# Optimization experiments

Measured on AMD Instinct MI355X. Metric: run time of the kernel, lower is better.

## Reference

```python
import jax, jax.numpy as jnp
import numpy as np

E = 8            # num experts
CAP_FACTOR = 1.5
K_THRESH = 0.8
BAL_ALPHA = 0.005
REG_ALPHA = 1e-6
BN_EPS = 1e-5
POOL = 16


def setup_inputs() -> dict:
    key = jax.random.key(0)
    ks = jax.random.split(key, 8)
    B, H, L, D = 128, 1024, 512, 1024
    return {
        "x": jax.random.normal(ks[0], (B, H, L), jnp.float32),
        "conv_w": jax.random.normal(ks[1], (64, H, 3), jnp.float32) / np.float32(np.sqrt(3 * H)),
        "conv_b": jnp.zeros((64,), jnp.float32),
        "bn_gamma": jnp.ones((64 * POOL,), jnp.float32),
        "bn_beta": jnp.zeros((64 * POOL,), jnp.float32),
        "fc1_w": jax.random.normal(ks[2], (128, 64 * POOL), jnp.float32) / np.float32(np.sqrt(64 * POOL)),
        "fc1_b": jnp.zeros((128,), jnp.float32),
        "fc2_w": jax.random.normal(ks[3], (E, 128), jnp.float32) / np.float32(np.sqrt(128)),
        "fc2_b": jnp.zeros((E,), jnp.float32),
        "exp_w": jax.random.normal(ks[4], (E, H, D), jnp.float32) / np.float32(np.sqrt(H)),
        "exp_b": jnp.zeros((E, D), jnp.float32),
    }


def _forward(x, conv_w, conv_b, bn_gamma, bn_beta, fc1_w, fc1_b, fc2_w, fc2_b, exp_w, exp_b):
    B, H, L = x.shape
    # ---- router: Conv1d(H->64,k=3,p=1) -> GELU -> AdaptiveAvgPool1d(16) -> Flatten -> BN -> FC -> GELU -> FC -> softmax
    h = jax.lax.conv_general_dilated(x, conv_w, (1,), ((1, 1),),
                                     dimension_numbers=("NCH", "OIH", "NCH"))
    h = jax.nn.gelu(h + conv_b[None, :, None], approximate=False)          # [B,64,L]; torch GELU is exact erf
    h = h.reshape(B, 64, POOL, L // POOL).mean(-1).reshape(B, 64 * POOL)   # adaptive avg pool (L%16==0) + flatten
    mu, var = h.mean(0), h.var(0)                                          # training-mode (Sync)BatchNorm: batch stats
    h = (h - mu) / jnp.sqrt(var + BN_EPS) * bn_gamma + bn_beta
    h = jax.nn.gelu(h @ fc1_w.T + fc1_b, approximate=False)
    rw = jax.nn.softmax(h @ fc2_w.T + fc2_b, axis=1)                       # [B,E]; expert dropout = identity (eval)
    # ---- dynamic k: smallest k s.t. cumsum of sorted probs > threshold; only max over batch is used
    topk_w, topk_idx = jax.lax.top_k(rw, E)                                # full descending sort
    cum = jnp.cumsum(topk_w, axis=1)
    over = cum > K_THRESH
    k_per = jnp.where(jnp.any(over, axis=1), jnp.argmax(over, axis=1) + 1, E)
    max_k = jnp.max(jnp.clip(k_per, 1, E))
    col_valid = jnp.arange(E)[None, :] < max_k                             # broadcast [B,E]; cols >= max_k unused
    assign = jnp.where(col_valid, topk_idx, -1)
    # ---- capacity enforcement: per expert keep the `capacity` highest-weight assignments, drop the rest (-1)
    capacity = max(1, int(B * CAP_FACTOR / E))
    flat_idx, flat_w = assign.reshape(-1), topk_w.reshape(-1)              # row-major [B*E], matches torch flatten

    def keep_for_expert(e):
        m = flat_idx == e
        order = jnp.argsort(-jnp.where(m, flat_w, -jnp.inf))               # descending within expert e
        ranks = jnp.zeros_like(order).at[order].set(jnp.arange(order.shape[0]))
        return m & (ranks < capacity)

    keep = jax.vmap(keep_for_expert)(jnp.arange(E))                        # [E, B*E]
    counts = keep.sum(axis=1).astype(jnp.float32)                          # == bincount of valid final indices
    final_idx = jnp.where(jnp.any(keep, axis=0), flat_idx, -1).reshape(B, E)
    # ---- experts: mean-pool over length, per-expert Linear(H->D); gather each sample's selected experts
    pooled = x.mean(axis=2)                                                # [B,H]
    y = jnp.einsum("bh,ehd->bed", pooled, exp_w) + exp_b[None]             # [B,E,D] all-expert outputs
    outputs = jnp.take_along_axis(y, jnp.clip(final_idx, 0)[..., None], axis=1)
    outputs = jnp.where(final_idx[..., None] >= 0, outputs, 0.0)           # dropped slots contribute zeros
    # ---- combine: softmax over the max_k slots; dropped (-1) slots enter softmax with logit 0, as in torch
    logits = jnp.where(col_valid, topk_w * (final_idx >= 0), -jnp.inf)
    norm_w = jax.nn.softmax(logits, axis=1)                                # [B,E]
    pooler = jnp.einsum("bkd,bk->bd", outputs, norm_w)                     # [B,D]
    # ---- losses / stats
    usage = rw.mean(0)
    reg = jnp.sum(exp_w * exp_w) + jnp.sum(exp_b * exp_b)                  # sum ||param||_2^2 over expert params
    added_loss = BAL_ALPHA * jnp.var(usage, ddof=1) + REG_ALPHA * reg      # torch.var is unbiased
    return pooler, added_loss, usage, counts


def reference(x, conv_w, conv_b, bn_gamma, bn_beta, fc1_w, fc1_b, fc2_w, fc2_b, exp_w, exp_b):
    return _forward(x, conv_w, conv_b, bn_gamma, bn_beta, fc1_w, fc1_b, fc2_w, fc2_b, exp_w, exp_b)
```

## Files before the change

kernel.cpp:

```cpp
#include <hip/hip_runtime.h>
#include <hip/hip_bf16.h>
#include <math.h>

#define NB 128
#define NH 1024
#define NL 512
#define OC 64
#define NE 8
#define ND 1024
#define CAPACITY 24

static const size_t WS_PART  = 0;
static const size_t WS_WSEP  = 1048576;
static const size_t WS_PXT   = 2097152;
static const size_t WS_HPOOL = 2228224;
static const size_t WS_SCALE = 2359296;
static const size_t WS_SHIFT = 2360320;
static const size_t WS_A1    = 2361344;
static const size_t WS_TKW   = 2377728;
static const size_t WS_TKI   = 2378752;
static const size_t WS_USAGE = 2379784;
static const size_t WS_VARU  = 2379792;
static const size_t WS_REG   = 2379793;
static const size_t WS_CNT   = 2379794;
static const size_t WS_WMAT  = 2380832;
static const size_t WS_RW    = 2381856;
static const size_t WS_KP    = 2382880;

typedef __attribute__((ext_vector_type(8))) short bf16x8;
typedef __attribute__((ext_vector_type(4))) float f32x4;

__device__ __forceinline__ float gelu_exact(float v) {
    return 0.5f * v * (1.0f + erff(v * 0.70710678118654752440f));
}

__device__ __forceinline__ unsigned short f2bf_rne(float f) {
    unsigned int u = __float_as_uint(f);
    unsigned int r = u + 0x7FFFu + ((u >> 16) & 1u);
    return (unsigned short)(r >> 16);
}
__device__ __forceinline__ float bf2f(unsigned short h) {
    return __uint_as_float(((unsigned int)h) << 16);
}

__device__ __forceinline__ unsigned cvtpk_bf16(float a, float b) {
    unsigned r;
    asm("v_cvt_pk_bf16_f32 %0, %1, %2" : "=v"(r) : "v"(a), "v"(b));
    return r;
}

__global__ __launch_bounds__(256) void k_wsplit(const float* __restrict__ cw, float* __restrict__ ws)
{
    if (blockIdx.x == 0 && threadIdx.x == 0) ws[WS_REG] = 0.0f;
    unsigned short* wsep = (unsigned short*)(ws + WS_WSEP);
    int i = blockIdx.x * 256 + threadIdx.x;
    float v = cw[i];
    int j = i % 3;
    int t = i / 3;
    int h = t & 1023;
    int o = t >> 10;
    int it = h >> 5;
    int h5 = h & 31;
    int e = h5 & 7;
    int lane = (o & 15) | ((h5 >> 3) << 4);
    int mt = (o >> 4) & 3;
    unsigned short hi = f2bf_rne(v);
    unsigned short lo = f2bf_rne(v - bf2f(hi));
    size_t base = ((size_t)((it * 3 + j) * 4 + mt) * 2) * 512 + lane * 8 + e;
    wsep[base] = hi;
    wsep[base + 512] = lo;
}

__device__ __forceinline__ void cvt_unit(unsigned int* X, int lq, int h4,
                                         const float4* v, float* sh)
{
    sh[0] = sh[1] = sh[2] = sh[3] = 0.f;
#pragma unroll
    for (int i = 0; i < 4; ++i) {
        float a0 = ((const float*)&v[0])[i];
        float a1 = ((const float*)&v[1])[i];
        float a2 = ((const float*)&v[2])[i];
        float a3 = ((const float*)&v[3])[i];
        sh[0] += a0; sh[1] += a1; sh[2] += a2; sh[3] += a3;
        unsigned h01 = cvtpk_bf16(a0, a1);
        unsigned h23 = cvtpk_bf16(a2, a3);
        float r0 = a0 - __uint_as_float(h01 << 16);
        float r1 = a1 - __uint_as_float(h01 & 0xFFFF0000u);
        float r2 = a2 - __uint_as_float(h23 << 16);
        float r3 = a3 - __uint_as_float(h23 & 0xFFFF0000u);
        unsigned l01 = cvtpk_bf16(r0, r1);
        unsigned l23 = cvtpk_bf16(r2, r3);
        int r = lq * 4 + i;
        unsigned int* dst = X + r * 34 + ((2 * h4) ^ ((r & 3) << 2));
        *(uint2*)dst = make_uint2(h01, h23);
        *(uint2*)(dst + 16) = make_uint2(l01, l23);
    }
}

__global__ __launch_bounds__(256, 2) void k_convmfma(const float* __restrict__ x,
                                                     const float* __restrict__ cb,
                                                     float* __restrict__ ws)
{
    __shared__ unsigned int Xb[2][136 * 34];
    __shared__ float xs2[3][128];
    __shared__ float scb[64];

    const int lc = blockIdx.x, b = blockIdx.y;
    const int l0 = lc * 128;
    const int tid = threadIdx.x;
    const int wv = tid >> 6, lane = tid & 63;
    const int h4 = tid & 7;
    const int lqi = 1 + (tid >> 3);
    const bool has_halo = (tid < 16);
    const int lqh = (tid < 8) ? 0 : 33;
    const bool halo_ok = (tid < 8) ? (lc > 0) : (lc < 3);

    const unsigned short* wsg = (const unsigned short*)(ws + WS_WSEP);
    const float* xbase = x + (size_t)b * (NH * NL);
    float* poolp = ws + WS_PART + ((size_t)(lc * 128 + b)) * 1024;

    if (tid < 64) scb[tid] = cb[tid];

    f32x4 acc[4][2];
#pragma unroll
    for (int mt = 0; mt < 4; ++mt)
#pragma unroll
        for (int nt = 0; nt < 2; ++nt) acc[mt][nt] = (f32x4){0.f, 0.f, 0.f, 0.f};

    float4 xA[4], hA[4], xB[4], hB[4];

    auto xload = [&](int itL, float4* xc, float4* hc) {
        const int hn = itL * 32;
        const float* p = xbase + (size_t)(hn + h4 * 4) * NL + (l0 - 4 + lqi * 4);
#pragma unroll
        for (int jj = 0; jj < 4; ++jj) xc[jj] = *(const float4*)(p + jj * NL);
        if (has_halo) {
            int gl = l0 - 4 + lqh * 4;
#pragma unroll
            for (int jj = 0; jj < 4; ++jj)
                hc[jj] = halo_ok ? *(const float4*)(xbase + (size_t)(hn + h4 * 4 + jj) * NL + gl)
                                 : make_float4(0.f, 0.f, 0.f, 0.f);
        }
    };

    auto body = [&](int it, float4* xc, float4* hc) {
        unsigned int* Xw = Xb[it & 1];
        bf16x8 Ar[3][4][2];
        {
            const unsigned short* abase = wsg + (size_t)it * 12288 + lane * 8;
#pragma unroll
            for (int j = 0; j < 3; ++j)
#pragma unroll
                for (int mt = 0; mt < 4; ++mt) {
                    Ar[j][mt][0] = *(const bf16x8*)(abase + (size_t)(j * 8 + mt * 2) * 512);
                    Ar[j][mt][1] = *(const bf16x8*)(abase + (size_t)(j * 8 + mt * 2 + 1) * 512);
                }
        }
        {
            float sh[4];
            cvt_unit(Xw, lqi, h4, xc, sh);
#pragma unroll
            for (int jj = 0; jj < 4; ++jj) {
                float s = sh[jj];
                s += __shfl_xor(s, 8, 64);
                s += __shfl_xor(s, 16, 64);
                s += __shfl_xor(s, 32, 64);
                if ((lane >> 3) == 0) xs2[it % 3][wv * 32 + h4 * 4 + jj] = s;
            }
            if (has_halo) { float d[4]; cvt_unit(Xw, lqh, h4, hc, d); }
        }
        __syncthreads();
        if (it > 0 && tid < 32) {
            const float* S = xs2[(it - 1) % 3];
            poolp[(it - 1) * 32 + tid] = S[tid] + S[32 + tid] + S[64 + tid] + S[96 + tid];
        }
        if (it < 30) xload(it + 2, xc, hc);
        const int g4 = (lane >> 4) << 2;
#pragma unroll
        for (int j = 0; j < 3; ++j) {
            bf16x8 Bh[2], Bl[2];
#pragma unroll
            for (int nt = 0; nt < 2; ++nt) {
                int rx = 3 + j + wv * 32 + nt * 16 + (lane & 15);
                const unsigned int* bp = Xw + rx * 34 + (g4 ^ ((rx & 3) << 2));
                Bh[nt] = *(const bf16x8*)bp;
                Bl[nt] = *(const bf16x8*)(bp + 16);
            }
#pragma unroll
            for (int mt = 0; mt < 4; ++mt)
#pragma unroll
                for (int nt = 0; nt < 2; ++nt) {
                    acc[mt][nt] = __builtin_amdgcn_mfma_f32_16x16x32_bf16(Ar[j][mt][0], Bh[nt], acc[mt][nt], 0, 0, 0);
                    acc[mt][nt] = __builtin_amdgcn_mfma_f32_16x16x32_bf16(Ar[j][mt][0], Bl[nt], acc[mt][nt], 0, 0, 0);
                    acc[mt][nt] = __builtin_amdgcn_mfma_f32_16x16x32_bf16(Ar[j][mt][1], Bh[nt], acc[mt][nt], 0, 0, 0);
                }
        }
    };

    xload(0, xA, hA);
    xload(1, xB, hB);

    for (int it2 = 0; it2 < 32; it2 += 2) {
        body(it2, xA, hA);
        body(it2 + 1, xB, hB);
    }
    if (tid < 32) {
        const float* S = xs2[31 % 3];
        poolp[31 * 32 + tid] = S[tid] + S[32 + tid] + S[64 + tid] + S[96 + tid];
    }

    {
        const int g = lane >> 4, cidx = lane & 15;
#pragma unroll
        for (int mt = 0; mt < 4; ++mt) {
            float s[4];
#pragma unroll
            for (int r = 0; r < 4; ++r) {
                int o = mt * 16 + g * 4 + r;
                float bo = scb[o];
                s[r] = gelu_exact(acc[mt][0][r] + bo) + gelu_exact(acc[mt][1][r] + bo);
            }
#pragma unroll
            for (int m = 1; m < 16; m <<= 1) {
#pragma unroll
                for (int r = 0; r < 4; ++r) s[r] += __shfl_xor(s[r], m, 64);
            }
            if (cidx == 0) {
#pragma unroll
                for (int r = 0; r < 4; ++r) {
                    int o = mt * 16 + g * 4 + r;
                    ws[WS_HPOOL + (size_t)b * 1024 + o * 16 + lc * 4 + wv] = s[r] * (1.0f / 32.0f);
                }
            }
        }
    }
}

__global__ __launch_bounds__(256) void k_mid(const float* __restrict__ g,
                                             const float* __restrict__ bet,
                                             float* __restrict__ ws)
{
    int bx = blockIdx.x;
    if (bx < 512) {
        int id = bx * 256 + threadIdx.x;
        int b = id >> 10, h = id & 1023;
        float s = 0.0f;
#pragma unroll
        for (int lcc = 0; lcc < 4; lcc++) s += ws[WS_PART + ((size_t)(lcc * 128 + b)) * 1024 + h];
        ws[WS_PXT + (size_t)h * 128 + b] = s * (1.0f / 512.0f);
    } else {
        int f = (bx - 512) * 256 + threadIdx.x;
        const float* hp = ws + WS_HPOOL;
        float s = 0.0f;
        for (int b = 0; b < 128; b++) s += hp[(size_t)b * 1024 + f];
        float mu = s * (1.0f / 128.0f);
        float v = 0.0f;
        for (int b = 0; b < 128; b++) { float d = hp[(size_t)b * 1024 + f] - mu; v += d * d; }
        float var = v * (1.0f / 128.0f);
        float sc = g[f] / sqrtf(var + 1e-5f);
        ws[WS_SCALE + f] = sc;
        ws[WS_SHIFT + f] = bet[f] - mu * sc;
    }
}

__global__ __launch_bounds__(256) void k_fused(const float* __restrict__ w1,
                                               const float* __restrict__ b1,
                                               const float* __restrict__ w2,
                                               const float* __restrict__ b2,
                                               const float* __restrict__ ew,
                                               const float* __restrict__ eb,
                                               float* __restrict__ ws)
{
    __shared__ float smem[6400];
    const int bx = blockIdx.x;
    const int tid = threadIdx.x;

    if (bx < 256) {
        float* a_s = smem;
        float* b_s = smem + 4096;
        float* red2 = smem + 6144;
        const int e = bx >> 5, dt = (bx >> 1) & 15, ks = bx & 1;
        const int tb = tid >> 3, td = tid & 7;
        float acc[4][8];
#pragma unroll
        for (int i = 0; i < 4; i++)
#pragma unroll
            for (int j = 0; j < 8; j++) acc[i][j] = 0.0f;
        float ssq = 0.0f;

        const float* pxt = ws + WS_PXT;
        for (int kt = 0; kt < 512; kt += 32) {
            __syncthreads();
            for (int idx = tid; idx < 4096; idx += 256) {
                int kk = idx >> 7, bb = idx & 127;
                a_s[kk * 128 + bb] = pxt[(size_t)(ks * 512 + kt + kk) * 128 + bb];
            }
            for (int idx = tid; idx < 2048; idx += 256) {
                int kk = idx >> 6, d = idx & 63;
                float v = ew[(size_t)e * 1048576 + (size_t)(ks * 512 + kt + kk) * 1024 + dt * 64 + d];
                b_s[kk * 64 + d] = v;
                ssq += v * v;
            }
            __syncthreads();
#pragma unroll 4
            for (int kk = 0; kk < 32; kk++) {
                float4 av = *(const float4*)&a_s[kk * 128 + tb * 4];
                float4 b0 = *(const float4*)&b_s[kk * 64 + td * 8];
                float4 b1v = *(const float4*)&b_s[kk * 64 + td * 8 + 4];
                float aa[4] = {av.x, av.y, av.z, av.w};
                float bb4[8] = {b0.x, b0.y, b0.z, b0.w, b1v.x, b1v.y, b1v.z, b1v.w};
#pragma unroll
                for (int i = 0; i < 4; i++)
#pragma unroll
                    for (int j = 0; j < 8; j++) acc[i][j] = fmaf(aa[i], bb4[j], acc[i][j]);
            }
        }
        float* outp = ws + WS_PART + ((size_t)(ks * 8 + e) * 128) * 1024 + dt * 64;
#pragma unroll
        for (int i = 0; i < 4; i++) {
            int bb = tb * 4 + i;
            *(float4*)(outp + (size_t)bb * 1024 + td * 8) =
                make_float4(acc[i][0], acc[i][1], acc[i][2], acc[i][3]);
            *(float4*)(outp + (size_t)bb * 1024 + td * 8 + 4) =
                make_float4(acc[i][4], acc[i][5], acc[i][6], acc[i][7]);
        }
        if (bx == 0)
            for (int i = tid; i < 8192; i += 256) { float v = eb[i]; ssq += v * v; }
        red2[tid] = ssq;
        __syncthreads();
        for (int off = 128; off > 0; off >>= 1) {
            if (tid < off) red2[tid] += red2[tid + off];
            __syncthreads();
        }
        if (tid == 0) atomicAdd(ws + WS_REG, red2[0]);
    } else {
        float* hb  = smem;
        float* red = smem + 1024;
        float* ha  = smem + 1280;
        float* w2s = smem + 1408;
        float* lg  = smem + 2432;
        const int b = bx - 256;
        const float* hp = ws + WS_HPOOL + (size_t)b * 1024;
        for (int k = tid; k < 1024; k += 256)
            hb[k] = hp[k] * ws[WS_SCALE + k] + ws[WS_SHIFT + k];
        for (int i = tid; i < 1024; i += 256) w2s[i] = w2[i];
        __syncthreads();
        int o = tid & 127, kh = tid >> 7;
        const float4* wrp = (const float4*)(w1 + (size_t)o * 1024 + kh * 512);
        const float* hx = hb + kh * 512;
        float acc = 0.0f;
#pragma unroll 4
        for (int k = 0; k < 128; k++) {
            float4 w = wrp[k];
            acc = fmaf(hx[4 * k], w.x, acc);     acc = fmaf(hx[4 * k + 1], w.y, acc);
            acc = fmaf(hx[4 * k + 2], w.z, acc); acc = fmaf(hx[4 * k + 3], w.w, acc);
        }
        red[tid] = acc;
        __syncthreads();
        if (tid < 128)
            ha[tid] = gelu_exact(red[tid] + red[tid + 128] + b1[tid]);
        __syncthreads();
        if (tid < 8) {
            float a2 = b2[tid];
            for (int k = 0; k < 128; k++) a2 = fmaf(ha[k], w2s[tid * 128 + k], a2);
            lg[tid] = a2;
        }
        __syncthreads();
        if (tid == 0) {
            float rw[8];
            float m = -1e30f;
#pragma unroll
            for (int e = 0; e < 8; e++) m = fmaxf(m, lg[e]);
            float s = 0.0f;
#pragma unroll
            for (int e = 0; e < 8; e++) { rw[e] = expf(lg[e] - m); s += rw[e]; }
            float inv = 1.0f / s;
#pragma unroll
            for (int e = 0; e < 8; e++) { rw[e] *= inv; ws[WS_RW + b * 8 + e] = rw[e]; }
            float tw[8]; int ti[8]; unsigned used = 0;
#pragma unroll
            for (int r = 0; r < 8; r++) {
                float bv = -1e30f; int bi = 0;
#pragma unroll
                for (int e = 0; e < 8; e++) {
                    bool take = !((used >> e) & 1u) && (rw[e] > bv);
                    bv = take ? rw[e] : bv;
                    bi = take ? e : bi;
                }
                used |= (1u << bi);
                tw[r] = bv; ti[r] = bi;
            }
            float cum = 0.0f; int kp = 8;
#pragma unroll
            for (int r = 0; r < 8; r++) {
                cum += tw[r];
                if (cum > 0.8f) { kp = r + 1; break; }
            }
#pragma unroll
            for (int r = 0; r < 8; r++) {
                ws[WS_TKW + b * 8 + r] = tw[r];
                ((int*)ws)[WS_TKI + b * 8 + r] = ti[r];
            }
            ((int*)ws)[WS_KP + b] = kp;
        }
    }
}

__global__ __launch_bounds__(128) void k_route(float* __restrict__ ws)
{
    __shared__ float tkw_s[1024];
    __shared__ int   tki_s[1024];
    __shared__ int   keep_s[1024];
    __shared__ float wv_s[128];
    __shared__ int   sv_s[128];
    __shared__ float usg[8];
    __shared__ int   cnt_s[8];
    __shared__ int   mk;

    const int tid = threadIdx.x;
    const int b = tid;
    if (tid == 0) mk = 0;
    if (tid < 8) cnt_s[tid] = 0;
    __syncthreads();
    atomicMax(&mk, ((const int*)ws)[WS_KP + b]);
#pragma unroll
    for (int r = 0; r < 8; r++) {
        tkw_s[b * 8 + r] = ws[WS_TKW + b * 8 + r];
        tki_s[b * 8 + r] = ((const int*)ws)[WS_TKI + b * 8 + r];
    }
    __syncthreads();
    const int maxk = mk;

    if (tid < 8) {
        float s2 = 0.0f;
        for (int bb = 0; bb < 128; bb++) s2 += ws[WS_RW + bb * 8 + tid];
        float u = s2 * (1.0f / 128.0f);
        usg[tid] = u;
        ws[WS_USAGE + tid] = u;
    }
    __syncthreads();
    if (tid == 0) {
        float mu = 0.0f;
#pragma unroll
        for (int e = 0; e < 8; e++) mu += usg[e];
        mu *= (1.0f / 8.0f);
        float v = 0.0f;
#pragma unroll
        for (int e = 0; e < 8; e++) { float d = usg[e] - mu; v += d * d; }
        ws[WS_VARU] = v * (1.0f / 7.0f);
    }

    for (int e = 0; e < 8; ++e) {
        float myw = 0.0f; int mys = -1;
        for (int k = 0; k < maxk; k++)
            if (tki_s[b * 8 + k] == e) { myw = tkw_s[b * 8 + k]; mys = b * 8 + k; }
        wv_s[b] = myw; sv_s[b] = mys;
        __syncthreads();
        if (mys >= 0) {
            int rank = 0;
            for (int b2 = 0; b2 < 128; b2++) {
                int s2 = sv_s[b2];
                if (s2 >= 0) {
                    float w2v = wv_s[b2];
                    if (w2v > myw || (w2v == myw && s2 < mys)) rank++;
                }
            }
            int kept = (rank < CAPACITY) ? 1 : 0;
            keep_s[mys] = kept;
            if (kept) atomicAdd(&cnt_s[e], 1);
        }
        __syncthreads();
    }
    if (tid < 8) ws[WS_CNT + tid] = (float)cnt_s[tid];

    float lv[8]; int kept[8]; int idx[8];
#pragma unroll
    for (int k = 0; k < 8; k++) {
        if (k < maxk) {
            kept[k] = keep_s[b * 8 + k];
            idx[k] = tki_s[b * 8 + k];
            lv[k] = kept[k] ? tkw_s[b * 8 + k] : 0.0f;
        } else { kept[k] = 0; idx[k] = -1; lv[k] = -1e30f; }
    }
    float mx = -1e30f;
#pragma unroll
    for (int k = 0; k < 8; k++) if (k < maxk) mx = fmaxf(mx, lv[k]);
    float s3 = 0.0f; float ev[8];
#pragma unroll
    for (int k = 0; k < 8; k++) { ev[k] = (k < maxk) ? expf(lv[k] - mx) : 0.0f; s3 += ev[k]; }
    float inv3 = 1.0f / s3;
    float Wr[8] = {0, 0, 0, 0, 0, 0, 0, 0};
#pragma unroll
    for (int k = 0; k < 8; k++) {
        if (kept[k]) {
            float v = ev[k] * inv3;
#pragma unroll
            for (int e = 0; e < 8; e++) Wr[e] += (idx[k] == e) ? v : 0.0f;
        }
    }
#pragma unroll
    for (int e = 0; e < 8; e++) ws[WS_WMAT + b * 8 + e] = Wr[e];
}

__global__ __launch_bounds__(256) void k_final(const float* __restrict__ eb,
                                               const float* __restrict__ ws,
                                               float* __restrict__ out)
{
    int id = blockIdx.x * 256 + threadIdx.x;
    int b = id >> 10, d = id & 1023;
    const float* wm = ws + WS_WMAT + b * 8;
    const float* Y = ws + WS_PART;
    float s = 0.0f;
#pragma unroll
    for (int e = 0; e < 8; e++) {
        float y = Y[((size_t)e * 128 + b) * 1024 + d]
                + Y[((size_t)(8 + e) * 128 + b) * 1024 + d]
                + eb[(size_t)e * 1024 + d];
        s += wm[e] * y;
    }
    out[id] = s;
    if (blockIdx.x == 0) {
        int t = threadIdx.x;
        if (t == 0) out[131072] = 0.005f * ws[WS_VARU] + 1e-6f * ws[WS_REG];
        else if (t >= 1 && t < 9)  out[131072 + t] = ws[WS_USAGE + t - 1];
        else if (t >= 9 && t < 17) out[131072 + t] = ws[WS_CNT + t - 9];
    }
}

extern "C" void kernel_launch(void* const* d_in, const int* in_sizes, int n_in,
                              void* d_out, int out_size, void* d_ws, size_t ws_size,
                              hipStream_t stream)
{
    const float* x   = (const float*)d_in[0];
    const float* cw  = (const float*)d_in[1];
    const float* cb  = (const float*)d_in[2];
    const float* bng = (const float*)d_in[3];
    const float* bnb = (const float*)d_in[4];
    const float* f1w = (const float*)d_in[5];
    const float* f1b = (const float*)d_in[6];
    const float* f2w = (const float*)d_in[7];
    const float* f2b = (const float*)d_in[8];
    const float* ew  = (const float*)d_in[9];
    const float* eb  = (const float*)d_in[10];
    float* ws  = (float*)d_ws;
    float* out = (float*)d_out;

    k_wsplit  <<<768, 256, 0, stream>>>(cw, ws);
    k_convmfma<<<dim3(4, 128), 256, 0, stream>>>(x, cb, ws);
    k_mid     <<<516, 256, 0, stream>>>(bng, bnb, ws);
    k_fused   <<<384, 256, 0, stream>>>(f1w, f1b, f2w, f2b, ew, eb, ws);
    k_route   <<<1, 128, 0, stream>>>(ws);
    k_final   <<<512, 256, 0, stream>>>(eb, ws, out);
}
```

Baseline: 316.0 us.

## Widen conv tile to 256 positions with 512 threads and LDS-staged weights

The conv MFMA kernel now runs blocks of 512 threads (8 waves), each covering 256 sequence positions instead of 128, which halves the number of blocks and the halo overhead. Split-bf16 weight fragments are staged into double-buffered LDS through direct global-to-LDS loads rather than being loaded into registers by every wave. The x loading layout is also reorganized so each wave reads contiguous rows. The cost is more LDS per block and fewer blocks, which may limit occupancy and parallelism (256 blocks in total).

```diff
diff --git a/kernel.cpp b/kernel.cpp
--- a/kernel.cpp
+++ b/kernel.cpp
@@ -16,7 +16,6 @@
 static const size_t WS_HPOOL = 2228224;
 static const size_t WS_SCALE = 2359296;
 static const size_t WS_SHIFT = 2360320;
-static const size_t WS_A1    = 2361344;
 static const size_t WS_TKW   = 2377728;
 static const size_t WS_TKI   = 2378752;
 static const size_t WS_USAGE = 2379784;
@@ -47,6 +46,13 @@
     unsigned r;
     asm("v_cvt_pk_bf16_f32 %0, %1, %2" : "=v"(r) : "v"(a), "v"(b));
     return r;
+}
+
+__device__ __forceinline__ void gload_lds16(const void* gsrc, void* ldst) {
+    __builtin_amdgcn_global_load_lds(
+        (const __attribute__((address_space(1))) void*)gsrc,
+        (__attribute__((address_space(3))) void*)ldst,
+        16, 0, 0);
 }
 
 __global__ __launch_bounds__(256) void k_wsplit(const float* __restrict__ cw, float* __restrict__ ws)
@@ -71,49 +77,19 @@
     wsep[base + 512] = lo;
 }
 
-__device__ __forceinline__ void cvt_unit(unsigned int* X, int lq, int h4,
-                                         const float4* v, float* sh)
-{
-    sh[0] = sh[1] = sh[2] = sh[3] = 0.f;
-#pragma unroll
-    for (int i = 0; i < 4; ++i) {
-        float a0 = ((const float*)&v[0])[i];
-        float a1 = ((const float*)&v[1])[i];
-        float a2 = ((const float*)&v[2])[i];
-        float a3 = ((const float*)&v[3])[i];
-        sh[0] += a0; sh[1] += a1; sh[2] += a2; sh[3] += a3;
-        unsigned h01 = cvtpk_bf16(a0, a1);
-        unsigned h23 = cvtpk_bf16(a2, a3);
-        float r0 = a0 - __uint_as_float(h01 << 16);
-        float r1 = a1 - __uint_as_float(h01 & 0xFFFF0000u);
-        float r2 = a2 - __uint_as_float(h23 << 16);
-        float r3 = a3 - __uint_as_float(h23 & 0xFFFF0000u);
-        unsigned l01 = cvtpk_bf16(r0, r1);
-        unsigned l23 = cvtpk_bf16(r2, r3);
-        int r = lq * 4 + i;
-        unsigned int* dst = X + r * 34 + ((2 * h4) ^ ((r & 3) << 2));
-        *(uint2*)dst = make_uint2(h01, h23);
-        *(uint2*)(dst + 16) = make_uint2(l01, l23);
-    }
-}
-
-__global__ __launch_bounds__(256, 2) void k_convmfma(const float* __restrict__ x,
+__global__ __launch_bounds__(512, 2) void k_convmfma(const float* __restrict__ x,
                                                      const float* __restrict__ cb,
                                                      float* __restrict__ ws)
 {
-    __shared__ unsigned int Xb[2][136 * 34];
-    __shared__ float xs2[3][128];
+    __shared__ unsigned int Xb[2][264 * 34];
+    __shared__ unsigned short Ab[2][12288];
+    __shared__ float xs2[2][256];
     __shared__ float scb[64];
 
     const int lc = blockIdx.x, b = blockIdx.y;
-    const int l0 = lc * 128;
+    const int l0 = lc * 256;
     const int tid = threadIdx.x;
-    const int wv = tid >> 6, lane = tid & 63;
-    const int h4 = tid & 7;
-    const int lqi = 1 + (tid >> 3);
-    const bool has_halo = (tid < 16);
-    const int lqh = (tid < 8) ? 0 : 33;
-    const bool halo_ok = (tid < 8) ? (lc > 0) : (lc < 3);
+    const int w = tid >> 6, lane = tid & 63;
 
     const unsigned short* wsg = (const unsigned short*)(ws + WS_WSEP);
     const float* xbase = x + (size_t)b * (NH * NL);
@@ -127,86 +103,129 @@
 #pragma unroll
         for (int nt = 0; nt < 2; ++nt) acc[mt][nt] = (f32x4){0.f, 0.f, 0.f, 0.f};
 
-    float4 xA[4], hA[4], xB[4], hB[4];
-
-    auto xload = [&](int itL, float4* xc, float4* hc) {
-        const int hn = itL * 32;
-        const float* p = xbase + (size_t)(hn + h4 * 4) * NL + (l0 - 4 + lqi * 4);
-#pragma unroll
-        for (int jj = 0; jj < 4; ++jj) xc[jj] = *(const float4*)(p + jj * NL);
-        if (has_halo) {
-            int gl = l0 - 4 + lqh * 4;
-#pragma unroll
-            for (int jj = 0; jj < 4; ++jj)
-                hc[jj] = halo_ok ? *(const float4*)(xbase + (size_t)(hn + h4 * 4 + jj) * NL + gl)
-                                 : make_float4(0.f, 0.f, 0.f, 0.f);
+    float4 xrA[4], xrB[4]; float4 hrA, hrB;
+    const int hrow = lane & 3, hside = (lane >> 2) & 1;
+    const bool hact = (lane < 8);
+    const bool hok = hside ? (lc == 0) : (lc == 1);
+
+    auto xload = [&](int itL, float4* xr, float4& hr) {
+        const int ht = itL * 32;
+        const float* pr = xbase + (size_t)(ht + 4 * w) * NL + (l0 + 4 * lane);
+#pragma unroll
+        for (int rr = 0; rr < 4; ++rr) xr[rr] = *(const float4*)(pr + rr * NL);
+        if (hact) {
+            int gl = hside ? (l0 + 256) : (l0 - 4);
+            hr = hok ? *(const float4*)(xbase + (size_t)(ht + 4 * w + hrow) * NL + gl)
+                     : make_float4(0.f, 0.f, 0.f, 0.f);
         }
     };
 
-    auto body = [&](int it, float4* xc, float4* hc) {
-        unsigned int* Xw = Xb[it & 1];
-        bf16x8 Ar[3][4][2];
-        {
-            const unsigned short* abase = wsg + (size_t)it * 12288 + lane * 8;
-#pragma unroll
-            for (int j = 0; j < 3; ++j)
-#pragma unroll
-                for (int mt = 0; mt < 4; ++mt) {
-                    Ar[j][mt][0] = *(const bf16x8*)(abase + (size_t)(j * 8 + mt * 2) * 512);
-                    Ar[j][mt][1] = *(const bf16x8*)(abase + (size_t)(j * 8 + mt * 2 + 1) * 512);
+    auto adma = [&](int itL) {
+        const unsigned short* src = wsg + (size_t)itL * 12288;
+        unsigned short* dst = Ab[itL & 1];
+#pragma unroll
+        for (int c = 0; c < 3; ++c)
+            gload_lds16(src + (size_t)(c * 512 + tid) * 8, dst + (size_t)(c * 512 + tid) * 8);
+    };
+
+    auto cvt = [&](int itL, const float4* xr, const float4& hr) {
+        unsigned int* X = Xb[itL & 1];
+        float ps0 = 0.f, ps1 = 0.f, ps2 = 0.f, ps3 = 0.f;
+#pragma unroll
+        for (int i = 0; i < 4; ++i) {
+            float a0 = ((const float*)&xr[0])[i];
+            float a1 = ((const float*)&xr[1])[i];
+            float a2 = ((const float*)&xr[2])[i];
+            float a3 = ((const float*)&xr[3])[i];
+            ps0 += a0; ps1 += a1; ps2 += a2; ps3 += a3;
+            unsigned h01 = cvtpk_bf16(a0, a1);
+            unsigned h23 = cvtpk_bf16(a2, a3);
+            float r0 = a0 - __uint_as_float(h01 << 16);
+            float r1 = a1 - __uint_as_float(h01 & 0xFFFF0000u);
+            float r2 = a2 - __uint_as_float(h23 << 16);
+            float r3 = a3 - __uint_as_float(h23 & 0xFFFF0000u);
+            unsigned l01 = cvtpk_bf16(r0, r1);
+            unsigned l23 = cvtpk_bf16(r2, r3);
+            int r = 4 + lane * 4 + i;
+            int sw = (r & 3) << 2;
+            unsigned int* row = X + r * 34;
+            *(uint2*)(row + ((2 * w) ^ sw)) = make_uint2(h01, h23);
+            *(uint2*)(row + 16 + ((2 * w) ^ sw)) = make_uint2(l01, l23);
+        }
+        float psv[4] = {ps0, ps1, ps2, ps3};
+#pragma unroll
+        for (int rr = 0; rr < 4; ++rr) {
+            float s = psv[rr];
+            s += __shfl_xor(s, 1, 64);
+            s += __shfl_xor(s, 2, 64);
+            s += __shfl_xor(s, 4, 64);
+            if ((lane & 7) == 0) xs2[itL & 1][w * 32 + (lane >> 3) * 4 + rr] = s;
+        }
+        if (hact) {
+#pragma unroll
+            for (int i = 0; i < 4; ++i) {
+                float a = ((const float*)&hr)[i];
+                float ap = __shfl_xor(a, 1, 64);
+                int r = (hside ? 260 : 0) + i;
+                int sw = (r & 3) << 2;
+                unsigned h01 = cvtpk_bf16(a, ap);
+                float r0 = a - __uint_as_float(h01 << 16);
+                float r1 = ap - __uint_as_float(h01 & 0xFFFF0000u);
+                unsigned l01 = cvtpk_bf16(r0, r1);
+                if ((hrow & 1) == 0) {
+                    int d = 2 * w + (hrow >> 1);
+                    X[r * 34 + (d ^ sw)] = h01;
+                    X[r * 34 + 16 + (d ^ sw)] = l01;
                 }
-        }
-        {
-            float sh[4];
-            cvt_unit(Xw, lqi, h4, xc, sh);
-#pragma unroll
-            for (int jj = 0; jj < 4; ++jj) {
-                float s = sh[jj];
-                s += __shfl_xor(s, 8, 64);
-                s += __shfl_xor(s, 16, 64);
-                s += __shfl_xor(s, 32, 64);
-                if ((lane >> 3) == 0) xs2[it % 3][wv * 32 + h4 * 4 + jj] = s;
-            }
-            if (has_halo) { float d[4]; cvt_unit(Xw, lqh, h4, hc, d); }
-        }
-        __syncthreads();
-        if (it > 0 && tid < 32) {
-            const float* S = xs2[(it - 1) % 3];
-            poolp[(it - 1) * 32 + tid] = S[tid] + S[32 + tid] + S[64 + tid] + S[96 + tid];
-        }
-        if (it < 30) xload(it + 2, xc, hc);
-        const int g4 = (lane >> 4) << 2;
-#pragma unroll
-        for (int j = 0; j < 3; ++j) {
-            bf16x8 Bh[2], Bl[2];
+            }
+        }
+    };
+
+    auto mfmaJ = [&](int itL, int j) {
+        const unsigned short* A = Ab[itL & 1] + j * 4096 + lane * 8;
+        const unsigned int* X = Xb[itL & 1];
+        bf16x8 Bh[2], Bl[2];
+#pragma unroll
+        for (int nt = 0; nt < 2; ++nt) {
+            int rx = 3 + j + w * 32 + nt * 16 + (lane & 15);
+            const unsigned int* bp = X + rx * 34 + (((lane >> 4) << 2) ^ ((rx & 3) << 2));
+            Bh[nt] = *(const bf16x8*)bp;
+            Bl[nt] = *(const bf16x8*)(bp + 16);
+        }
+#pragma unroll
+        for (int mt = 0; mt < 4; ++mt) {
+            bf16x8 Ah = *(const bf16x8*)(A + mt * 1024);
+            bf16x8 Al = *(const bf16x8*)(A + mt * 1024 + 512);
 #pragma unroll
             for (int nt = 0; nt < 2; ++nt) {
-                int rx = 3 + j + wv * 32 + nt * 16 + (lane & 15);
-                const unsigned int* bp = Xw + rx * 34 + (g4 ^ ((rx & 3) << 2));
-                Bh[nt] = *(const bf16x8*)bp;
-                Bl[nt] = *(const bf16x8*)(bp + 16);
-            }
-#pragma unroll
-            for (int mt = 0; mt < 4; ++mt)
-#pragma unroll
-                for (int nt = 0; nt < 2; ++nt) {
-                    acc[mt][nt] = __builtin_amdgcn_mfma_f32_16x16x32_bf16(Ar[j][mt][0], Bh[nt], acc[mt][nt], 0, 0, 0);
-                    acc[mt][nt] = __builtin_amdgcn_mfma_f32_16x16x32_bf16(Ar[j][mt][0], Bl[nt], acc[mt][nt], 0, 0, 0);
-                    acc[mt][nt] = __builtin_amdgcn_mfma_f32_16x16x32_bf16(Ar[j][mt][1], Bh[nt], acc[mt][nt], 0, 0, 0);
-                }
+                acc[mt][nt] = __builtin_amdgcn_mfma_f32_16x16x32_bf16(Ah, Bh[nt], acc[mt][nt], 0, 0, 0);
+                acc[mt][nt] = __builtin_amdgcn_mfma_f32_16x16x32_bf16(Ah, Bl[nt], acc[mt][nt], 0, 0, 0);
+                acc[mt][nt] = __builtin_amdgcn_mfma_f32_16x16x32_bf16(Al, Bh[nt], acc[mt][nt], 0, 0, 0);
+            }
         }
     };
 
-    xload(0, xA, hA);
-    xload(1, xB, hB);
-
-    for (int it2 = 0; it2 < 32; it2 += 2) {
-        body(it2, xA, hA);
-        body(it2 + 1, xB, hB);
-    }
-    if (tid < 32) {
-        const float* S = xs2[31 % 3];
-        poolp[31 * 32 + tid] = S[tid] + S[32 + tid] + S[64 + tid] + S[96 + tid];
+    adma(0);
+    xload(0, xrA, hrA);
+    xload(1, xrB, hrB);
+
+    for (int it = 0; it < 32; ++it) {
+        if (it & 1) cvt(it, xrB, hrB); else cvt(it, xrA, hrA);
+        __syncthreads();
+        if (tid < 32) {
+            const float* S = xs2[it & 1];
+            float s = 0.f;
+#pragma unroll
+            for (int g = 0; g < 8; ++g) s += S[(tid >> 2) * 32 + g * 4 + (tid & 3)];
+            poolp[it * 32 + tid] = s;
+        }
+        if (it < 30) {
+            if (it & 1) xload(it + 2, xrB, hrB); else xload(it + 2, xrA, hrA);
+        }
+        if (it < 31) adma(it + 1);
+        mfmaJ(it, 0);
+        mfmaJ(it, 1);
+        mfmaJ(it, 2);
     }
 
     {
@@ -229,7 +248,7 @@
 #pragma unroll
                 for (int r = 0; r < 4; ++r) {
                     int o = mt * 16 + g * 4 + r;
-                    ws[WS_HPOOL + (size_t)b * 1024 + o * 16 + lc * 4 + wv] = s[r] * (1.0f / 32.0f);
+                    ws[WS_HPOOL + (size_t)b * 1024 + o * 16 + lc * 8 + w] = s[r] * (1.0f / 32.0f);
                 }
             }
         }
@@ -246,7 +265,7 @@
         int b = id >> 10, h = id & 1023;
         float s = 0.0f;
 #pragma unroll
-        for (int lcc = 0; lcc < 4; lcc++) s += ws[WS_PART + ((size_t)(lcc * 128 + b)) * 1024 + h];
+        for (int lcc = 0; lcc < 2; lcc++) s += ws[WS_PART + ((size_t)(lcc * 128 + b)) * 1024 + h];
         ws[WS_PXT + (size_t)h * 128 + b] = s * (1.0f / 512.0f);
     } else {
         int f = (bx - 512) * 256 + threadIdx.x;
@@ -546,7 +565,7 @@
     float* out = (float*)d_out;
 
     k_wsplit  <<<768, 256, 0, stream>>>(cw, ws);
-    k_convmfma<<<dim3(4, 128), 256, 0, stream>>>(x, cb, ws);
+    k_convmfma<<<dim3(2, 128), 512, 0, stream>>>(x, cb, ws);
     k_mid     <<<516, 256, 0, stream>>>(bng, bnb, ws);
     k_fused   <<<384, 256, 0, stream>>>(f1w, f1b, f2w, f2b, ew, eb, ws);
     k_route   <<<1, 128, 0, stream>>>(ws);
```

New measurement: 353.8 us. +11.9%, slower.
